# Kernel tuning notes

Measured on AMD Instinct MI355X. Metric: run time of the kernel, lower is better.

## Reference

```python
import jax, jax.numpy as jnp
import numpy as np

R, B, S, H, E, P = 8, 16, 512, 1024, 32, 4  # roles, batch, seq(=max_seq_len=char_len), hidden, entities, spans/entity


def setup_inputs() -> dict:
    key = jax.random.key(0)
    ks = jax.random.split(key, 12)
    w = 0.02
    return {
        "role_labels": jax.random.randint(ks[0], (R, B), 0, S),
        "summar_role_embedding": jax.random.normal(ks[1], (R, B, S, H), jnp.float32),
        "token_embedding": jax.random.normal(ks[2], (B, S, H), jnp.float32),
        "entities_embedding": jax.random.normal(ks[3], (B, S, H), jnp.float32),
        "token_mask": jnp.ones((B, S), jnp.float32),
        "entity_mask": jnp.ones((B, S), jnp.float32),
        # padded ragged spans: sort (start,end) so start<=end; empty spans write nothing
        "entity_spans": jnp.sort(jax.random.randint(ks[4], (B, E, P, 2), 0, S), axis=-1),
        # -1 encodes Python None entries in the original ragged maps
        "char2token": jax.random.randint(ks[5], (B, S), -1, S),
        "entity2token": jax.random.randint(ks[6], (B, S), -1, E),
        "single_w": jax.random.normal(ks[7], (3 * H, 1), jnp.float32) * w,
        "single_b": jnp.zeros((1,), jnp.float32),
        "multi_w": jax.random.normal(ks[8], (3 * H, 1), jnp.float32) * w,
        "multi_b": jnp.zeros((1,), jnp.float32),
        "answer_w": jax.random.normal(ks[9], (2 * H, H), jnp.float32) * w,
        "answer_b": jnp.zeros((H,), jnp.float32),
    }


def reference(role_labels, summar_role_embedding, token_embedding, entities_embedding,
              token_mask, entity_mask, entity_spans, char2token, entity2token,
              single_w, single_b, multi_w, multi_b, answer_w, answer_b):
    Bd, Sd, Hd = token_embedding.shape
    Ed = entity_spans.shape[1]
    brow = jnp.arange(Bd)[:, None]
    cvalid = char2token >= 0
    cidx = jnp.where(cvalid, char2token, 0)
    evalid = entity2token >= 0
    eidx = jnp.where(evalid, entity2token, 0)
    pos = jnp.arange(Sd)[None, None, None, :]  # [1,1,1,S]
    # span coverage mask [B,E,P,S]; assumes non-overlapping gold spans (matches sequential writes)
    cover = ((pos >= entity_spans[..., 0:1]) & (pos < entity_spans[..., 1:2])).astype(token_embedding.dtype)
    mask_sum = token_mask.sum()

    def step(pre_answer, xs):
        sr_emb, labels = xs
        s_logit = jnp.concatenate([sr_emb, token_embedding, pre_answer], -1) @ single_w + single_b  # [B,S,1]
        m_logit = jnp.concatenate([sr_emb, entities_embedding, pre_answer], -1) @ multi_w + multi_b
        # nn.Softmax() with no dim on a 3D tensor uses legacy dim=0 (batch axis)
        s_pred = jax.nn.softmax(s_logit, axis=0)[..., 0]  # [B,S]
        m_pred = jax.nn.softmax(m_logit, axis=0)[..., 0]
        # scatter-add char scores onto token positions / entity ids
        pred_token_ids = jnp.zeros((Bd, Sd), s_pred.dtype).at[brow, cidx].add(jnp.where(cvalid, s_pred, 0.0))
        entity_scores = jnp.zeros((Bd, Ed), m_pred.dtype).at[brow, eidx].add(jnp.where(evalid, m_pred, 0.0))
        # broadcast entity score over its spans
        pred_entity_ids = jnp.einsum('beps,be->bs', cover, entity_scores)
        merged = jnp.maximum(pred_token_ids, pred_entity_ids)  # max-merge [B,S]
        # gather merged scores back to char positions
        arg_emb = jnp.where(cvalid, jnp.take_along_axis(merged, cidx, axis=1), 0.0)[..., None]  # [B,S,1]
        curr = token_embedding * arg_emb
        new_pre = jnp.concatenate([curr, pre_answer], -1) @ answer_w + answer_b
        # CrossEntropyLoss(merged [B,C=S], labels [B]) -> scalar mean, then * token_mask.sum()
        nll = -jnp.take_along_axis(jax.nn.log_softmax(merged, -1), labels[:, None], axis=1).mean()
        return new_pre, (merged, nll * mask_sum)

    pre0 = jnp.zeros_like(token_embedding)
    _, (pred_arg_ids, losses) = jax.lax.scan(step, pre0, (summar_role_embedding, role_labels))
    return losses.sum(), pred_arg_ids
```

## Files before the change

### kernel.cpp

```cpp
#include <hip/hip_runtime.h>
#include <stdint.h>

#define R_ 8
#define B_ 16
#define S_ 512
#define H_ 1024
#define E_ 32
#define P_ 4
#define M_ (B_*S_)

__device__ __forceinline__ float dot4(float4 a, float4 b){
  return a.x*b.x + a.y*b.y + a.z*b.z + a.w*b.w;
}

__device__ __forceinline__ void group_barrier(int* cnt, int nblk){
  __syncthreads();
  if (threadIdx.x == 0){
    __threadfence();
    __hip_atomic_fetch_add(cnt, 1, __ATOMIC_RELEASE, __HIP_MEMORY_SCOPE_AGENT);
    while (__hip_atomic_load(cnt, __ATOMIC_ACQUIRE, __HIP_MEMORY_SCOPE_AGENT) < nblk)
      __builtin_amdgcn_s_sleep(8);
    __threadfence();
  }
  __syncthreads();
}

__global__ __launch_bounds__(256) void vec_chain_kernel(
    int k, const float* __restrict__ aw, const float* __restrict__ ab,
    const float* __restrict__ sw, const float* __restrict__ mw,
    float* __restrict__ a_s, float* __restrict__ a_m,
    float* __restrict__ V, float* __restrict__ betas)
{
  int w = (int)((blockIdx.x * blockDim.x + threadIdx.x) >> 6);
  int lane = threadIdx.x & 63;
  const float* as_k = (k == 0) ? (sw + 2*H_) : (a_s + (size_t)k*H_);
  const float* am_k = (k == 0) ? (mw + 2*H_) : (a_m + (size_t)k*H_);
  if (w < H_){
    const float* w1 = aw + (size_t)w * H_;
    const float* w2 = aw + (size_t)(H_ + w) * H_;
    float vs = 0.f, vm = 0.f, ns = 0.f, nm = 0.f;
    #pragma unroll
    for (int i = 0; i < 4; i++){
      int c = i*256 + lane*4;
      float4 r1 = *(const float4*)(w1 + c);
      float4 r2 = *(const float4*)(w2 + c);
      float4 xs = *(const float4*)(as_k + c);
      float4 xm = *(const float4*)(am_k + c);
      vs += dot4(r1, xs); vm += dot4(r1, xm);
      ns += dot4(r2, xs); nm += dot4(r2, xm);
    }
    #pragma unroll
    for (int m = 32; m >= 1; m >>= 1){
      vs += __shfl_xor(vs, m, 64); vm += __shfl_xor(vm, m, 64);
      ns += __shfl_xor(ns, m, 64); nm += __shfl_xor(nm, m, 64);
    }
    if (lane == 0){
      V[(size_t)k*H_ + w]       = vs;
      V[(size_t)(7 + k)*H_ + w] = vm;
      a_s[(size_t)(k+1)*H_ + w] = ns;
      a_m[(size_t)(k+1)*H_ + w] = nm;
    }
  } else if (w == H_ || w == H_ + 1){
    const float* av = (w == H_) ? as_k : am_k;
    float d = 0.f;
    #pragma unroll
    for (int i = 0; i < 4; i++){
      int c = i*256 + lane*4;
      d += dot4(*(const float4*)(ab + c), *(const float4*)(av + c));
    }
    #pragma unroll
    for (int m = 32; m >= 1; m >>= 1) d += __shfl_xor(d, m, 64);
    if (lane == 0) betas[(w == H_ ? 0 : 8) + k] = d;
  }
}

__global__ __launch_bounds__(256, 6) void dots_all_kernel(
    const float* __restrict__ sr, const float* __restrict__ tok,
    const float* __restrict__ ent, const float* __restrict__ sw,
    const float* __restrict__ mw, const float* __restrict__ V,
    const float* __restrict__ tmask,
    float* __restrict__ sr_s, float* __restrict__ sr_m,
    float* __restrict__ tok_s, float* __restrict__ ent_m,
    float* __restrict__ G, float* __restrict__ PS,
    float* __restrict__ msum, float* __restrict__ out)
{
  const int gtid = blockIdx.x * 256 + threadIdx.x;
  const int gw   = gtid >> 6;
  const int lane = threadIdx.x & 63;
  const int co   = lane * 4;

  if (gtid < 32768) ((float4*)PS)[gtid] = make_float4(0.f,0.f,0.f,0.f);
  if (gw == 0){
    float s = 0.f;
    #pragma unroll
    for (int i = 0; i < 32; i++){
      float4 v = ((const float4*)tmask)[i*64 + lane];
      s += v.x + v.y + v.z + v.w;
    }
    #pragma unroll
    for (int m = 32; m >= 1; m >>= 1) s += __shfl_xor(s, m, 64);
    if (lane == 0){ msum[0] = s; out[0] = 0.f; }
  }

  {
    float4 ws4[4], wm4[4];
    #pragma unroll
    for (int i = 0; i < 4; i++){
      ws4[i] = *(const float4*)(sw + i*256 + co);
      wm4[i] = *(const float4*)(mw + i*256 + co);
    }
    #pragma unroll
    for (int it = 0; it < 8; ++it){
      int w = gw + it*8192;
      const float* rp = sr + (size_t)w * H_;
      float a0 = 0.f, a1 = 0.f;
      #pragma unroll
      for (int i = 0; i < 4; i++){
        float4 v = *(const float4*)(rp + i*256 + co);
        a0 += dot4(v, ws4[i]);
        a1 += dot4(v, wm4[i]);
      }
      #pragma unroll
      for (int m = 32; m >= 1; m >>= 1){
        a0 += __shfl_xor(a0,m,64); a1 += __shfl_xor(a1,m,64);
      }
      if (lane == 0){ sr_s[w] = a0; sr_m[w] = a1; }
    }
  }

  {
    const int h  = gw & 1;
    const int r0 = gw >> 1;
    if (h == 0){
      #pragma unroll
      for (int it = 0; it < 2; ++it){
        int rr = r0 + it*4096;
        const float* rp = tok + (size_t)rr * H_;
        float acc[8];
        #pragma unroll
        for (int q = 0; q < 8; q++) acc[q] = 0.f;
        #pragma unroll
        for (int i = 0; i < 4; i++){
          int c = i*256 + co;
          float4 v = *(const float4*)(rp + c);
          acc[0] += dot4(v, *(const float4*)(sw + H_ + c));
          #pragma unroll
          for (int q = 0; q < 7; q++)
            acc[q+1] += dot4(v, *(const float4*)(V + (size_t)q*H_ + c));
        }
        #pragma unroll
        for (int m = 32; m >= 1; m >>= 1)
          #pragma unroll
          for (int q = 0; q < 8; q++) acc[q] += __shfl_xor(acc[q],m,64);
        if (lane == 0){
          tok_s[rr] = acc[0];
          #pragma unroll
          for (int q = 0; q < 7; q++) G[(size_t)q*M_ + rr] = acc[q+1];
        }
      }
    } else {
      #pragma unroll
      for (int it = 0; it < 2; ++it){
        int rr = r0 + it*4096;
        const float* rp = tok + (size_t)rr * H_;
        float acc[7];
        #pragma unroll
        for (int q = 0; q < 7; q++) acc[q] = 0.f;
        #pragma unroll
        for (int i = 0; i < 4; i++){
          int c = i*256 + co;
          float4 v = *(const float4*)(rp + c);
          #pragma unroll
          for (int q = 0; q < 7; q++)
            acc[q] += dot4(v, *(const float4*)(V + (size_t)(7+q)*H_ + c));
        }
        #pragma unroll
        for (int m = 32; m >= 1; m >>= 1)
          #pragma unroll
          for (int q = 0; q < 7; q++) acc[q] += __shfl_xor(acc[q],m,64);
        if (lane == 0){
          #pragma unroll
          for (int q = 0; q < 7; q++) G[(size_t)(7+q)*M_ + rr] = acc[q];
        }
      }
    }
  }

  {
    const float* rp = ent + (size_t)gw * H_;
    float a0 = 0.f;
    #pragma unroll
    for (int i = 0; i < 4; i++){
      float4 v = *(const float4*)(rp + i*256 + co);
      a0 += dot4(v, *(const float4*)(mw + H_ + i*256 + co));
    }
    #pragma unroll
    for (int m = 32; m >= 1; m >>= 1) a0 += __shfl_xor(a0,m,64);
    if (lane == 0) ent_m[gw] = a0;
  }
}

__global__ __launch_bounds__(512) void roles_kernel(
    const float* __restrict__ sr_s, const float* __restrict__ sr_m,
    const float* __restrict__ tok_s, const float* __restrict__ ent_m,
    const float* __restrict__ G, const float* __restrict__ betas,
    const float* __restrict__ sb, const float* __restrict__ mb,
    const int* __restrict__ c2t, const int* __restrict__ e2t,
    const int* __restrict__ spans, const int* __restrict__ labels,
    const float* __restrict__ msum, float* __restrict__ out,
    float* __restrict__ xlog, float* __restrict__ PS, int* bar)
{
  __shared__ float pta[S_];
  __shared__ float merged[S_];
  __shared__ float es[E_];
  __shared__ float red[8];
  __shared__ int   spn[E_*P_*2];
  const int b = blockIdx.x;
  const int t = threadIdx.x;
  const int bs = b*S_ + t;
  const int wid = t >> 6, lane = t & 63;

  if (t < E_*P_*2) spn[t] = spans[b*(E_*P_*2) + t];
  const int c_own = c2t[bs];
  const int e_own = e2t[bs];
  const float sb0 = sb[0], mb0 = mb[0];
  const float msumv = msum[0];
  const float tok_sv = tok_s[bs], ent_mv = ent_m[bs];
  float bsum_s = 0.f, bsum_m = 0.f;

  for (int r = 0; r < R_; ++r){
    pta[t] = 0.f;
    if (t < E_) es[t] = 0.f;

    float sl[B_], ml[B_];
    if (r == 0){
      #pragma unroll
      for (int bb = 0; bb < B_; bb++){
        int q = bb*S_ + t;
        sl[bb] = sr_s[q] + tok_s[q] + sb0;
        ml[bb] = sr_m[q] + ent_m[q] + mb0;
      }
    } else {
      const float* xc = xlog + (size_t)(r & 1) * (2*M_);
      #pragma unroll
      for (int bb = 0; bb < B_; bb++){
        sl[bb] = xc[bb*S_ + t];
        ml[bb] = xc[M_ + bb*S_ + t];
      }
    }
    float smax = -1e30f, mmax = -1e30f;
    #pragma unroll
    for (int bb = 0; bb < B_; bb++){ smax = fmaxf(smax, sl[bb]); mmax = fmaxf(mmax, ml[bb]); }
    float ssum = 0.f, msv = 0.f;
    #pragma unroll
    for (int bb = 0; bb < B_; bb++){ ssum += __expf(sl[bb]-smax); msv += __expf(ml[bb]-mmax); }
    float spv = __expf(sl[b]-smax) / ssum;
    float mpv = __expf(ml[b]-mmax) / msv;

    __syncthreads();
    if (c_own >= 0) atomicAdd(&pta[c_own], spv);
    if (e_own >= 0) atomicAdd(&es[e_own], mpv);
    __syncthreads();

    float pei = 0.f;
    #pragma unroll
    for (int e = 0; e < E_; e++){
      float sc = es[e];
      #pragma unroll
      for (int p = 0; p < P_; p++){
        int st = spn[e*8 + p*2], en = spn[e*8 + p*2 + 1];
        if (t >= st && t < en) pei += sc;
      }
    }
    float mg = fmaxf(pta[t], pei);
    merged[t] = mg;
    out[1 + (size_t)r*M_ + bs] = mg;
    __syncthreads();

    float ah_r = (c_own >= 0) ? merged[c_own] : 0.f;

    float mx = mg;
    #pragma unroll
    for (int k = 32; k >= 1; k >>= 1) mx = fmaxf(mx, __shfl_xor(mx, k, 64));
    if (lane == 0) red[wid] = mx;
    __syncthreads();
    float gmx = red[0];
    #pragma unroll
    for (int i = 1; i < 8; i++) gmx = fmaxf(gmx, red[i]);
    float se = __expf(mg - gmx);
    #pragma unroll
    for (int k = 32; k >= 1; k >>= 1) se += __shfl_xor(se, k, 64);
    __syncthreads();
    if (lane == 0) red[wid] = se;
    __syncthreads();
    if (t == 0){
      float tot = 0.f;
      #pragma unroll
      for (int i = 0; i < 8; i++) tot += red[i];
      float lse = gmx + __logf(tot);
      int lbl = labels[r*B_ + b];
      float nll = lse - merged[lbl];
      atomicAdd(out, nll * msumv * (1.0f/16.0f));
    }

    if (r < 7){
      bsum_s += betas[r]; bsum_m += betas[8 + r];
      float ps_next = 0.f, pm_next = 0.f;
      for (int q = r + 1; q <= 7; q++){
        float gs = G[(size_t)(q-1-r)*M_ + bs];
        float gm = G[(size_t)(7 + q-1-r)*M_ + bs];
        float ns = PS[((size_t)q*2 + 0)*M_ + bs] + ah_r * gs;
        float nm = PS[((size_t)q*2 + 1)*M_ + bs] + ah_r * gm;
        PS[((size_t)q*2 + 0)*M_ + bs] = ns;
        PS[((size_t)q*2 + 1)*M_ + bs] = nm;
        if (q == r + 1){ ps_next = ns; pm_next = nm; }
      }
      float xn = sr_s[(size_t)((r+1)*B_ + b)*S_ + t] + tok_sv + ps_next + sb0 + bsum_s;
      float yn = sr_m[(size_t)((r+1)*B_ + b)*S_ + t] + ent_mv + pm_next + mb0 + bsum_m;
      float* xn_buf = xlog + (size_t)((r+1) & 1) * (2*M_);
      xn_buf[bs] = xn;
      xn_buf[M_ + bs] = yn;
      group_barrier(&bar[r], 16);
    }
  }
}

extern "C" void kernel_launch(void* const* d_in, const int* in_sizes, int n_in,
                              void* d_out, int out_size, void* d_ws, size_t ws_size,
                              hipStream_t stream){
  (void)in_sizes; (void)n_in; (void)out_size; (void)ws_size;
  const int*   labels = (const int*)  d_in[0];
  const float* sr     = (const float*)d_in[1];
  const float* tok    = (const float*)d_in[2];
  const float* ent    = (const float*)d_in[3];
  const float* tmask  = (const float*)d_in[4];
  const int*   spans  = (const int*)  d_in[6];
  const int*   c2t    = (const int*)  d_in[7];
  const int*   e2t    = (const int*)  d_in[8];
  const float* sw     = (const float*)d_in[9];
  const float* sb     = (const float*)d_in[10];
  const float* mw     = (const float*)d_in[11];
  const float* mb     = (const float*)d_in[12];
  const float* aw     = (const float*)d_in[13];
  const float* ab     = (const float*)d_in[14];
  float* out = (float*)d_out;
  char*  ws  = (char*)d_ws;

  size_t o = 0;
  auto take = [&](size_t bytes){ size_t c = o; o += (bytes + 255) & ~(size_t)255; return c; };
  float* sr_s  = (float*)(ws + take((size_t)R_*B_*S_*4));
  float* sr_m  = (float*)(ws + take((size_t)R_*B_*S_*4));
  float* tok_s = (float*)(ws + take((size_t)B_*S_*4));
  float* ent_m = (float*)(ws + take((size_t)B_*S_*4));
  float* a_s   = (float*)(ws + take((size_t)8*H_*4));
  float* a_m   = (float*)(ws + take((size_t)8*H_*4));
  float* V     = (float*)(ws + take((size_t)14*H_*4));
  float* betas = (float*)(ws + take(64));
  float* G     = (float*)(ws + take((size_t)14*M_*4));
  float* PS    = (float*)(ws + take((size_t)8*2*M_*4));
  float* xlog  = (float*)(ws + take((size_t)2*2*M_*4));
  float* msum  = (float*)(ws + take(256));
  int*   bar   = (int*)  (ws + take(64));

  hipMemsetAsync(bar, 0, 64, stream);
  for (int k = 0; k < 7; k++)
    vec_chain_kernel<<<257, 256, 0, stream>>>(k, aw, ab, sw, mw, a_s, a_m, V, betas);
  dots_all_kernel<<<2048, 256, 0, stream>>>(sr, tok, ent, sw, mw, V, tmask,
                                            sr_s, sr_m, tok_s, ent_m, G, PS, msum, out);
  roles_kernel<<<16, 512, 0, stream>>>(sr_s, sr_m, tok_s, ent_m, G, betas,
                                       sb, mb, c2t, e2t, spans, labels, msum, out,
                                       xlog, PS, bar);
}
```

Baseline: 197.6 us.

## Split dots kernel into role-specialized blocks with LDS-staged summary reads

Restructures the big dot-product kernel so blocks are specialized: the first 1024 blocks stream summar_role_embedding rows into LDS via global_load_lds direct-to-LDS loads before dotting with the two weight vectors. The next 512 blocks handle token projections against the chain vectors, and the last 512 handle entity dots plus the PS zeroing and mask sum. Previously every block did a bit of all three phases. The intent is to improve memory streaming for the dominant summary read and to balance work per block. In exchange it adds 32KB LDS per block and extra barriers, which lower occupancy, and the phase-specialized blocks may finish unevenly.

```diff
diff --git a/kernel.cpp b/kernel.cpp
--- a/kernel.cpp
+++ b/kernel.cpp
@@ -8,6 +8,9 @@
 #define E_ 32
 #define P_ 4
 #define M_ (B_*S_)
+#define SRB2_ 1024
+#define TOKB_ 512
+#define ENTB_ 512
 
 __device__ __forceinline__ float dot4(float4 a, float4 b){
   return a.x*b.x + a.y*b.y + a.z*b.z + a.w*b.w;
@@ -74,7 +77,7 @@
   }
 }
 
-__global__ __launch_bounds__(256, 6) void dots_all_kernel(
+__global__ __launch_bounds__(256) void dots_staged_kernel(
     const float* __restrict__ sr, const float* __restrict__ tok,
     const float* __restrict__ ent, const float* __restrict__ sw,
     const float* __restrict__ mw, const float* __restrict__ V,
@@ -84,57 +87,57 @@
     float* __restrict__ G, float* __restrict__ PS,
     float* __restrict__ msum, float* __restrict__ out)
 {
-  const int gtid = blockIdx.x * 256 + threadIdx.x;
-  const int gw   = gtid >> 6;
+  __shared__ float lds[8*1024];
+  const int blk  = blockIdx.x;
   const int lane = threadIdx.x & 63;
+  const int lw   = threadIdx.x >> 6;
   const int co   = lane * 4;
 
-  if (gtid < 32768) ((float4*)PS)[gtid] = make_float4(0.f,0.f,0.f,0.f);
-  if (gw == 0){
-    float s = 0.f;
-    #pragma unroll
-    for (int i = 0; i < 32; i++){
-      float4 v = ((const float4*)tmask)[i*64 + lane];
-      s += v.x + v.y + v.z + v.w;
-    }
-    #pragma unroll
-    for (int m = 32; m >= 1; m >>= 1) s += __shfl_xor(s, m, 64);
-    if (lane == 0){ msum[0] = s; out[0] = 0.f; }
-  }
-
-  {
+  if (blk < SRB2_){
     float4 ws4[4], wm4[4];
     #pragma unroll
     for (int i = 0; i < 4; i++){
       ws4[i] = *(const float4*)(sw + i*256 + co);
       wm4[i] = *(const float4*)(mw + i*256 + co);
     }
-    #pragma unroll
     for (int it = 0; it < 8; ++it){
-      int w = gw + it*8192;
-      const float* rp = sr + (size_t)w * H_;
-      float a0 = 0.f, a1 = 0.f;
-      #pragma unroll
-      for (int i = 0; i < 4; i++){
-        float4 v = *(const float4*)(rp + i*256 + co);
-        a0 += dot4(v, ws4[i]);
-        a1 += dot4(v, wm4[i]);
-      }
-      #pragma unroll
-      for (int m = 32; m >= 1; m >>= 1){
-        a0 += __shfl_xor(a0,m,64); a1 += __shfl_xor(a1,m,64);
-      }
-      if (lane == 0){ sr_s[w] = a0; sr_m[w] = a1; }
-    }
-  }
-
-  {
+      const int row0 = (blk + it*SRB2_) * 8;
+      #pragma unroll
+      for (int j = 0; j < 8; ++j){
+        int c = lw*8 + j;
+        int row = c >> 2, part = c & 3;
+        const float* gp = sr + (size_t)(row0 + row)*H_ + part*256 + lane*4;
+        float* lp = lds + row*1024 + part*256;
+        __builtin_amdgcn_global_load_lds(
+            (const __attribute__((address_space(1))) unsigned int*)gp,
+            (__attribute__((address_space(3))) unsigned int*)lp, 16, 0, 0);
+      }
+      __syncthreads();
+      #pragma unroll
+      for (int rr = 0; rr < 2; ++rr){
+        int row = lw*2 + rr;
+        float a0 = 0.f, a1 = 0.f;
+        #pragma unroll
+        for (int i = 0; i < 4; i++){
+          float4 v = *(const float4*)(lds + row*1024 + i*256 + co);
+          a0 += dot4(v, ws4[i]);
+          a1 += dot4(v, wm4[i]);
+        }
+        #pragma unroll
+        for (int m = 32; m >= 1; m >>= 1){
+          a0 += __shfl_xor(a0,m,64); a1 += __shfl_xor(a1,m,64);
+        }
+        if (lane == 0){ sr_s[row0 + row] = a0; sr_m[row0 + row] = a1; }
+      }
+      __syncthreads();
+    }
+  } else if (blk < SRB2_ + TOKB_){
+    const int gw = (blk - SRB2_)*4 + lw;
     const int h  = gw & 1;
     const int r0 = gw >> 1;
     if (h == 0){
-      #pragma unroll
-      for (int it = 0; it < 2; ++it){
-        int rr = r0 + it*4096;
+      for (int it = 0; it < 8; ++it){
+        int rr = r0 + it*1024;
         const float* rp = tok + (size_t)rr * H_;
         float acc[8];
         #pragma unroll
@@ -159,9 +162,8 @@
         }
       }
     } else {
-      #pragma unroll
-      for (int it = 0; it < 2; ++it){
-        int rr = r0 + it*4096;
+      for (int it = 0; it < 8; ++it){
+        int rr = r0 + it*1024;
         const float* rp = tok + (size_t)rr * H_;
         float acc[7];
         #pragma unroll
@@ -184,19 +186,37 @@
         }
       }
     }
-  }
-
-  {
-    const float* rp = ent + (size_t)gw * H_;
-    float a0 = 0.f;
-    #pragma unroll
-    for (int i = 0; i < 4; i++){
-      float4 v = *(const float4*)(rp + i*256 + co);
-      a0 += dot4(v, *(const float4*)(mw + H_ + i*256 + co));
-    }
-    #pragma unroll
-    for (int m = 32; m >= 1; m >>= 1) a0 += __shfl_xor(a0,m,64);
-    if (lane == 0) ent_m[gw] = a0;
+  } else {
+    const int eb = blk - SRB2_ - TOKB_;
+    const int gt = eb*256 + threadIdx.x;
+    if (gt < 32768) ((float4*)PS)[gt] = make_float4(0.f,0.f,0.f,0.f);
+    if (eb == 0 && lw == 0){
+      float s = 0.f;
+      #pragma unroll
+      for (int i = 0; i < 32; i++){
+        float4 v = ((const float4*)tmask)[i*64 + lane];
+        s += v.x + v.y + v.z + v.w;
+      }
+      #pragma unroll
+      for (int m = 32; m >= 1; m >>= 1) s += __shfl_xor(s, m, 64);
+      if (lane == 0){ msum[0] = s; out[0] = 0.f; }
+    }
+    const int ew = eb*4 + lw;
+    float4 wmh[4];
+    #pragma unroll
+    for (int i = 0; i < 4; i++) wmh[i] = *(const float4*)(mw + H_ + i*256 + co);
+    #pragma unroll
+    for (int it = 0; it < 4; ++it){
+      int rr = ew + it*2048;
+      const float* rp = ent + (size_t)rr * H_;
+      float a0 = 0.f;
+      #pragma unroll
+      for (int i = 0; i < 4; i++)
+        a0 += dot4(*(const float4*)(rp + i*256 + co), wmh[i]);
+      #pragma unroll
+      for (int m = 32; m >= 1; m >>= 1) a0 += __shfl_xor(a0,m,64);
+      if (lane == 0) ent_m[rr] = a0;
+    }
   }
 }
 
@@ -365,8 +385,8 @@
   hipMemsetAsync(bar, 0, 64, stream);
   for (int k = 0; k < 7; k++)
     vec_chain_kernel<<<257, 256, 0, stream>>>(k, aw, ab, sw, mw, a_s, a_m, V, betas);
-  dots_all_kernel<<<2048, 256, 0, stream>>>(sr, tok, ent, sw, mw, V, tmask,
-                                            sr_s, sr_m, tok_s, ent_m, G, PS, msum, out);
+  dots_staged_kernel<<<2048, 256, 0, stream>>>(sr, tok, ent, sw, mw, V, tmask,
+                                               sr_s, sr_m, tok_s, ent_m, G, PS, msum, out);
   roles_kernel<<<16, 512, 0, stream>>>(sr_s, sr_m, tok_s, ent_m, G, betas,
                                        sb, mb, c2t, e2t, spans, labels, msum, out,
                                        xlog, PS, bar);
```

New measurement: 171.6 us. -13.2%, faster.
